# Optimization experiments

Hardware: AMD Instinct MI355X
Metric: run time of the kernel (lower is better)

The kernel has to match this reference:

```python
import jax, jax.numpy as jnp
import numpy as np

K = 20  # neighbors

def _edgeconv(x, W, b):
    # x: [B, C, N]; W: [O, 2C]; b: [O]
    xt = jnp.swapaxes(x, 1, 2)                      # [B, N, C]
    # pairwise (negative squared) distance: -|xi|^2 - 2 xi.xj ... wait torch: -xx - inner - xx^T
    inner = -2.0 * jnp.einsum('bic,bjc->bij', xt, xt)   # [B, N, N]
    xx = jnp.sum(xt * xt, axis=-1)                       # [B, N]
    pd = -xx[:, None, :] - inner - xx[:, :, None]        # [B, N, N]
    _, idx = jax.lax.top_k(pd, K)                        # [B, N, K] nearest neighbors
    # gather neighbor features: feat[b,n,k,:] = xt[b, idx[b,n,k], :]
    feat = jnp.take_along_axis(xt[:, None, :, :],        # [B,1,N,C]
                               idx[:, :, :, None], axis=2)  # [B, N, K, C]
    center = xt[:, :, None, :]                           # [B, N, 1, C]
    edge = jnp.concatenate([feat - center,
                            jnp.broadcast_to(center, feat.shape)], axis=-1)  # [B,N,K,2C]
    # 1x1 conv == linear over channel dim, then LeakyReLU(0.2)
    h = jnp.einsum('bnkc,oc->bnko', edge, W) + b         # [B, N, K, O]
    h = jnp.where(h >= 0, h, 0.2 * h)
    out = jnp.max(h, axis=2)                             # [B, N, O] (max over neighbors)
    return jnp.swapaxes(out, 1, 2)                       # [B, O, N]

def setup_inputs() -> dict:
    key = jax.random.key(0)
    k1, k2, k3 = jax.random.split(key, 3)
    B, C, N, O = 8, 64, 4096, 128
    x = jax.random.normal(k1, (B, C, N), dtype=jnp.float32)
    W = jax.random.normal(k2, (O, 2 * C), dtype=jnp.float32) * (1.0 / np.sqrt(2 * C))
    b = jax.random.normal(k3, (O,), dtype=jnp.float32) * 0.01
    return {"x": x, "W": W, "b": b}

def reference(x, W, b):
    return _edgeconv(x, W, b)
```

## Files before the change

kernel.cpp:

```cpp
#include <hip/hip_runtime.h>

#define BB 8
#define CC 64
#define OO 128
#define NN 4096
#define KNN 20
#define NT 256
#define NG 64
#define RING 9
#define TRIG 5
#define SPLITW 192
#define WSPL 384
#define TILEB (16 * SPLITW * 2)

typedef short bf16x8 __attribute__((ext_vector_type(8)));
typedef float f32x4 __attribute__((ext_vector_type(4)));
typedef const __attribute__((address_space(1))) unsigned int* gas_ptr;
typedef __attribute__((address_space(3))) unsigned int* las_ptr;

#define REP20(F, P) F(P,0) F(P,1) F(P,2) F(P,3) F(P,4) F(P,5) F(P,6) F(P,7) \
    F(P,8) F(P,9) F(P,10) F(P,11) F(P,12) F(P,13) F(P,14) F(P,15) F(P,16)   \
    F(P,17) F(P,18) F(P,19)

#define TS_DECL(P,k) float P##m##k = 1e30f; int P##p##k = -1;
#define TS_REPL(P,k)                                                        \
  { const bool _h = (P##kpos == (k));                                       \
    P##m##k = _h ? _d : P##m##k;                                            \
    P##p##k = _h ? _j : P##p##k; }

#define TS_N(vd, xd, va, xa, vb, xb)                                        \
  { const bool _g = (vb) > (va); vd = _g ? (vb) : (va); xd = _g ? (xb) : (xa); }

#define TS_TREE(P)                                                          \
  { float t0,t1,t2,t3,t4,t5,t6,t7,t8,t9; int y0,y1,y2,y3,y4,y5,y6,y7,y8,y9; \
    TS_N(t0,y0, P##m0,0,  P##m1,1)   TS_N(t1,y1, P##m2,2,  P##m3,3)         \
    TS_N(t2,y2, P##m4,4,  P##m5,5)   TS_N(t3,y3, P##m6,6,  P##m7,7)         \
    TS_N(t4,y4, P##m8,8,  P##m9,9)   TS_N(t5,y5, P##m10,10, P##m11,11)      \
    TS_N(t6,y6, P##m12,12, P##m13,13) TS_N(t7,y7, P##m14,14, P##m15,15)     \
    TS_N(t8,y8, P##m16,16, P##m17,17) TS_N(t9,y9, P##m18,18, P##m19,19)     \
    float u0,u1,u2,u3,u4; int z0,z1,z2,z3,z4;                               \
    TS_N(u0,z0, t0,y0, t1,y1) TS_N(u1,z1, t2,y2, t3,y3)                     \
    TS_N(u2,z2, t4,y4, t5,y5) TS_N(u3,z3, t6,y6, t7,y7)                     \
    TS_N(u4,z4, t8,y8, t9,y9)                                               \
    float w0,w1; int q0,q1;                                                 \
    TS_N(w0,q0, u0,z0, u1,z1) TS_N(w1,q1, u2,z2, u3,z3)                     \
    float e0; int r0;                                                       \
    TS_N(e0,r0, w0,q0, w1,q1)                                               \
    TS_N(P##kmax, P##kpos, e0,r0, u4,z4) }

#define TS_INS(P, dval, jval)                                               \
  { const float _d = (dval); const int _j = (jval);                         \
    REP20(TS_REPL, P)                                                       \
    TS_TREE(P) }

#define RT_UPDATE                                                           \
  { const int _s1 = __builtin_amdgcn_ds_swizzle(__float_as_int(A_kmax), 0x101F); \
    const float _m1 = fminf(A_kmax, __int_as_float(_s1));                   \
    const int _s2 = __builtin_amdgcn_ds_swizzle(__float_as_int(_m1), 0x201F); \
    rt = fminf(_m1, __int_as_float(_s2)); }

#define MSW(a, b)                                                           \
  { const bool _s = (A_m##b < A_m##a) ||                                    \
                    ((A_m##b == A_m##a) && (A_p##b < A_p##a));              \
    const float _fa = _s ? A_m##b : A_m##a;                                 \
    const float _fb = _s ? A_m##a : A_m##b;                                 \
    const int _ia = _s ? A_p##b : A_p##a;                                   \
    const int _ib = _s ? A_p##a : A_p##b;                                   \
    A_m##a = _fa; A_m##b = _fb; A_p##a = _ia; A_p##b = _ib; }

#define SRND_E MSW(0,1) MSW(2,3) MSW(4,5) MSW(6,7) MSW(8,9) MSW(10,11)      \
    MSW(12,13) MSW(14,15) MSW(16,17) MSW(18,19)
#define SRND_O MSW(1,2) MSW(3,4) MSW(5,6) MSW(7,8) MSW(9,10) MSW(11,12)     \
    MSW(13,14) MSW(15,16) MSW(17,18)
#define SORT20 SRND_E SRND_O SRND_E SRND_O SRND_E SRND_O SRND_E SRND_O      \
    SRND_E SRND_O SRND_E SRND_O SRND_E SRND_O SRND_E SRND_O SRND_E SRND_O  \
    SRND_E SRND_O

__device__ __forceinline__ unsigned rne_bf16(float f) {
  const unsigned u = __float_as_uint(f);
  return (u + 0x7fffu + ((u >> 16) & 1u)) >> 16;
}

__global__ __launch_bounds__(128, 3) void xprep_kernel(
    const float* __restrict__ x, const float* __restrict__ W,
    float* __restrict__ xsq, unsigned short* __restrict__ xsp,
    unsigned short* __restrict__ Wsp) {
  const int b = blockIdx.y;
  const int n = blockIdx.x * 128 + threadIdx.x;

  if (b == 0) {
    const int t = threadIdx.x;
    const int o0 = blockIdx.x * 4;
#pragma unroll
    for (int oo = 0; oo < 4; ++oo) {
      const int o = o0 + oo;
      const float w = W[(size_t)o * (2 * CC) + t];
      const unsigned h = rne_bf16(w);
      const float r = w - __uint_as_float(h << 16);
      const unsigned m = rne_bf16(r);
      const float s = r - __uint_as_float(m << 16);
      const unsigned l = rne_bf16(s);
      unsigned short* row = Wsp + (size_t)o * WSPL;
      row[t] = (unsigned short)h;
      row[128 + t] = (unsigned short)m;
      row[256 + t] = (unsigned short)l;
    }
  }

  const float* xb = x + (size_t)b * CC * NN;

  float xr[CC];
  float sq = 0.f;
#pragma unroll
  for (int c = 0; c < CC; ++c) {
    xr[c] = xb[(size_t)c * NN + n];
    sq = fmaf(xr[c], xr[c], sq);
  }
  xsq[(size_t)b * NN + n] = sq;

  unsigned* srow = (unsigned*)(xsp + ((size_t)b * NN + n) * SPLITW);
#pragma unroll
  for (int c = 0; c < CC; c += 2) {
    const unsigned h0 = rne_bf16(xr[c]), h1 = rne_bf16(xr[c + 1]);
    const float r0 = xr[c] - __uint_as_float(h0 << 16);
    const float r1 = xr[c + 1] - __uint_as_float(h1 << 16);
    const unsigned m0 = rne_bf16(r0), m1 = rne_bf16(r1);
    const float s0 = r0 - __uint_as_float(m0 << 16);
    const float s1 = r1 - __uint_as_float(m1 << 16);
    const unsigned l0 = rne_bf16(s0), l1 = rne_bf16(s1);
    srow[c / 2] = h0 | (h1 << 16);
    srow[32 + c / 2] = m0 | (m1 << 16);
    srow[64 + c / 2] = l0 | (l1 << 16);
  }
}

#define MFMA6(ACC, B0, B1, B2, B3, B4, B5)                                  \
  f32x4 ACC;                                                                \
  { f32x4 a0 = {0.f,0.f,0.f,0.f}; f32x4 a1 = {0.f,0.f,0.f,0.f};             \
    f32x4 a2 = {0.f,0.f,0.f,0.f}; f32x4 a3 = {0.f,0.f,0.f,0.f};             \
    a0 = __builtin_amdgcn_mfma_f32_16x16x32_bf16(Ah0, B0, a0, 0, 0, 0);     \
    a1 = __builtin_amdgcn_mfma_f32_16x16x32_bf16(Ah1, B1, a1, 0, 0, 0);     \
    a2 = __builtin_amdgcn_mfma_f32_16x16x32_bf16(Ah0, B2, a2, 0, 0, 0);     \
    a3 = __builtin_amdgcn_mfma_f32_16x16x32_bf16(Ah1, B3, a3, 0, 0, 0);     \
    a0 = __builtin_amdgcn_mfma_f32_16x16x32_bf16(Am0, B0, a0, 0, 0, 0);     \
    a1 = __builtin_amdgcn_mfma_f32_16x16x32_bf16(Am1, B1, a1, 0, 0, 0);     \
    a2 = __builtin_amdgcn_mfma_f32_16x16x32_bf16(Ah0, B4, a2, 0, 0, 0);     \
    a3 = __builtin_amdgcn_mfma_f32_16x16x32_bf16(Ah1, B5, a3, 0, 0, 0);     \
    a0 = __builtin_amdgcn_mfma_f32_16x16x32_bf16(Al0, B0, a0, 0, 0, 0);     \
    a1 = __builtin_amdgcn_mfma_f32_16x16x32_bf16(Al1, B1, a1, 0, 0, 0);     \
    a2 = __builtin_amdgcn_mfma_f32_16x16x32_bf16(Am0, B2, a2, 0, 0, 0);     \
    a3 = __builtin_amdgcn_mfma_f32_16x16x32_bf16(Am1, B3, a3, 0, 0, 0);     \
    ACC = (a0 + a1) + (a2 + a3); }

#define STAGEG(G, BUF)                                                      \
  { const char* tb = (const char*)xspB + (size_t)(4 * (G) + wv) * TILEB + gof; \
    char* lb = (char*)(BUF) + wv * 6144;                                    \
    __builtin_amdgcn_global_load_lds((gas_ptr)(const void*)(tb), (las_ptr)(void*)(lb), 16, 0, 0); \
    __builtin_amdgcn_global_load_lds((gas_ptr)(const void*)(tb + 64), (las_ptr)(void*)(lb + 1024), 16, 0, 0); \
    __builtin_amdgcn_global_load_lds((gas_ptr)(const void*)(tb + 128), (las_ptr)(void*)(lb + 2048), 16, 0, 0); \
    __builtin_amdgcn_global_load_lds((gas_ptr)(const void*)(tb + 192), (las_ptr)(void*)(lb + 3072), 16, 0, 0); \
    __builtin_amdgcn_global_load_lds((gas_ptr)(const void*)(tb + 256), (las_ptr)(void*)(lb + 4096), 16, 0, 0); \
    __builtin_amdgcn_global_load_lds((gas_ptr)(const void*)(tb + 320), (las_ptr)(void*)(lb + 5120), 16, 0, 0); }

#define TILE_MFMA_L(LBUF, BUF)                                              \
  { const char* bb = (const char*)(LBUF) + c16;                             \
    const bf16x8 Bh0 = *(const bf16x8*)(bb + (q + 0) * 256);                \
    const bf16x8 Bh1 = *(const bf16x8*)(bb + (q + 4) * 256);                \
    const bf16x8 Bm0 = *(const bf16x8*)(bb + (q + 8) * 256);                \
    const bf16x8 Bm1 = *(const bf16x8*)(bb + (q + 12) * 256);               \
    const bf16x8 Bl0 = *(const bf16x8*)(bb + (q + 16) * 256);               \
    const bf16x8 Bl1 = *(const bf16x8*)(bb + (q + 20) * 256);               \
    f32x4 ac0 = {0.f, 0.f, 0.f, 0.f};                                       \
    f32x4 ac1 = {0.f, 0.f, 0.f, 0.f};                                       \
    f32x4 ac2 = {0.f, 0.f, 0.f, 0.f};                                       \
    f32x4 ac3 = {0.f, 0.f, 0.f, 0.f};                                       \
    ac0 = __builtin_amdgcn_mfma_f32_16x16x32_bf16(Ah0, Bh0, ac0, 0, 0, 0);  \
    ac1 = __builtin_amdgcn_mfma_f32_16x16x32_bf16(Ah1, Bh1, ac1, 0, 0, 0);  \
    ac2 = __builtin_amdgcn_mfma_f32_16x16x32_bf16(Ah0, Bm0, ac2, 0, 0, 0);  \
    ac3 = __builtin_amdgcn_mfma_f32_16x16x32_bf16(Ah1, Bm1, ac3, 0, 0, 0);  \
    ac0 = __builtin_amdgcn_mfma_f32_16x16x32_bf16(Am0, Bh0, ac0, 0, 0, 0);  \
    ac1 = __builtin_amdgcn_mfma_f32_16x16x32_bf16(Am1, Bh1, ac1, 0, 0, 0);  \
    ac2 = __builtin_amdgcn_mfma_f32_16x16x32_bf16(Ah0, Bl0, ac2, 0, 0, 0);  \
    ac3 = __builtin_amdgcn_mfma_f32_16x16x32_bf16(Ah1, Bl1, ac3, 0, 0, 0);  \
    ac0 = __builtin_amdgcn_mfma_f32_16x16x32_bf16(Al0, Bh0, ac0, 0, 0, 0);  \
    ac1 = __builtin_amdgcn_mfma_f32_16x16x32_bf16(Al1, Bh1, ac1, 0, 0, 0);  \
    ac2 = __builtin_amdgcn_mfma_f32_16x16x32_bf16(Am0, Bm0, ac2, 0, 0, 0);  \
    ac3 = __builtin_amdgcn_mfma_f32_16x16x32_bf16(Am1, Bm1, ac3, 0, 0, 0);  \
    const f32x4 acc = (ac0 + ac1) + (ac2 + ac3);                            \
    float* bw = &bounce[BUF][wv][0];                                        \
    bw[(q * 4 + 0) * 20 + c] = acc[0];                                      \
    bw[(q * 4 + 1) * 20 + c] = acc[1];                                      \
    bw[(q * 4 + 2) * 20 + c] = acc[2];                                      \
    bw[(q * 4 + 3) * 20 + c] = acc[3]; }

#define TILE_VALS(T, BUF)                                                   \
  const float* br = &bounce[BUF][wv][myrow * 20 + 4 * g];                   \
  const f32x4 dots = *(const f32x4*)br;                                     \
  const float4 xx = *(const float4*)(xsqb + (T) * 16 + 4 * g);              \
  const float d0 = fmaf(-2.f, dots[0], xx.x);                               \
  const float d1 = fmaf(-2.f, dots[1], xx.y);                               \
  const float d2 = fmaf(-2.f, dots[2], xx.z);                               \
  const float d3 = fmaf(-2.f, dots[3], xx.w);                               \
  const int jb = (T) * 16 + 4 * g;

#define TILE_SELF(T, BUF, K0, K1, K2, K3)                                   \
  { TILE_VALS(T, BUF)                                                       \
    A_m##K0 = d0; A_p##K0 = jb;                                             \
    A_m##K1 = d1; A_p##K1 = jb + 1;                                         \
    A_m##K2 = d2; A_p##K2 = jb + 2;                                         \
    A_m##K3 = d3; A_p##K3 = jb + 3; }

#define TILE_SEL(T, BUF)                                                    \
  { TILE_VALS(T, BUF)                                                       \
    if (d0 <= rt) { myring[cnt] = make_float2(d0, __int_as_float(jb)); ++cnt; } \
    if (d1 <= rt) { myring[cnt] = make_float2(d1, __int_as_float(jb + 1)); ++cnt; } \
    if (d2 <= rt) { myring[cnt] = make_float2(d2, __int_as_float(jb + 2)); ++cnt; } \
    if (d3 <= rt) { myring[cnt] = make_float2(d3, __int_as_float(jb + 3)); ++cnt; } \
    if (__ballot(cnt >= TRIG)) {                                            \
      for (int _k = 0; _k < cnt; ++_k) {                                    \
        const float2 e = myring[_k];                                        \
        if (e.x < A_kmax) { TS_INS(A_, e.x, __float_as_int(e.y)) }          \
      }                                                                     \
      cnt = 0;                                                              \
    }                                                                       \
    RT_UPDATE }

__global__ __launch_bounds__(256, 2) void knn_kernel(
    const unsigned short* __restrict__ xsp, const float* __restrict__ xsq,
    const unsigned short* __restrict__ Wsp, const float* __restrict__ bias,
    unsigned short* __restrict__ Ab16, float* __restrict__ Q,
    int* __restrict__ idxf) {
  __shared__ unsigned short Bbuf0[4 * TILEB / 2];
  __shared__ unsigned short Bbuf1[4 * TILEB / 2];
  __shared__ float bounce[2][4][16 * 20];
  __shared__ float2 ring[256][RING];

  const int b = blockIdx.y;
  const int wv = threadIdx.x >> 6;
  const int lane = threadIdx.x & 63;
  const int q = lane >> 4;
  const int c = lane & 15;
  const int c16 = c * 16;
  const int gof = c * 384 + q * 16;
  const int ibase = blockIdx.x * 64 + wv * 16;
  const int myrow = q * 4 + (c & 3);
  const int g = c >> 2;
  const int isel = ibase + myrow;

  const unsigned short* xspB = xsp + (size_t)b * NN * SPLITW;
  const float* xsqb = xsq + (size_t)b * NN;

  const unsigned short* arow = xspB + (size_t)(ibase + c) * SPLITW + q * 8;
  const bf16x8 Ah0 = *(const bf16x8*)(arow);
  const bf16x8 Ah1 = *(const bf16x8*)(arow + 32);
  const bf16x8 Am0 = *(const bf16x8*)(arow + 64);
  const bf16x8 Am1 = *(const bf16x8*)(arow + 96);
  const bf16x8 Al0 = *(const bf16x8*)(arow + 128);
  const bf16x8 Al1 = *(const bf16x8*)(arow + 160);

  REP20(TS_DECL, A_)
  float A_kmax = 1e30f; int A_kpos = 0;
  float rt = 1e30f;
  float2* myring = ring[threadIdx.x];
  int cnt = 0;

  STAGEG(0, Bbuf0)
  __syncthreads();
  STAGEG(1, Bbuf1)
  TILE_MFMA_L(Bbuf0 + 0 * 3072, 0)
  TILE_MFMA_L(Bbuf0 + 1 * 3072, 1) TILE_SELF(0, 0, 0, 1, 2, 3)
  TILE_MFMA_L(Bbuf0 + 2 * 3072, 0) TILE_SELF(1, 1, 4, 5, 6, 7)
  TILE_MFMA_L(Bbuf0 + 3 * 3072, 1) TILE_SELF(2, 0, 8, 9, 10, 11)
  __syncthreads();
  STAGEG(2, Bbuf0)
  TILE_MFMA_L(Bbuf1 + 0 * 3072, 0) TILE_SELF(3, 1, 12, 13, 14, 15)
  TILE_MFMA_L(Bbuf1 + 1 * 3072, 1) TILE_SELF(4, 0, 16, 17, 18, 19)
  TS_TREE(A_)
  RT_UPDATE
  TILE_MFMA_L(Bbuf1 + 2 * 3072, 0) TILE_SEL(5, 1)
  TILE_MFMA_L(Bbuf1 + 3 * 3072, 1) TILE_SEL(6, 0)
  __syncthreads();

  for (int G = 2; G < NG - 1; ++G) {
    unsigned short* cur = (G & 1) ? Bbuf1 : Bbuf0;
    unsigned short* nxt = (G & 1) ? Bbuf0 : Bbuf1;
    STAGEG(G + 1, nxt)
    const int t0 = 4 * G;
    TILE_MFMA_L(cur + 0 * 3072, 0) TILE_SEL(t0 - 1, 1)
    TILE_MFMA_L(cur + 1 * 3072, 1) TILE_SEL(t0, 0)
    TILE_MFMA_L(cur + 2 * 3072, 0) TILE_SEL(t0 + 1, 1)
    TILE_MFMA_L(cur + 3 * 3072, 1) TILE_SEL(t0 + 2, 0)
    __syncthreads();
  }

  TILE_MFMA_L(Bbuf1 + 0 * 3072, 0) TILE_SEL(251, 1)
  TILE_MFMA_L(Bbuf1 + 1 * 3072, 1) TILE_SEL(252, 0)
  TILE_MFMA_L(Bbuf1 + 2 * 3072, 0) TILE_SEL(253, 1)
  TILE_MFMA_L(Bbuf1 + 3 * 3072, 1) TILE_SEL(254, 0)
  TILE_SEL(255, 1)

  for (int _k = 0; _k < cnt; ++_k) {
    const float2 e = myring[_k];
    if (e.x < A_kmax) { TS_INS(A_, e.x, __float_as_int(e.y)) }
  }

  __syncthreads();
  {
    SORT20
    float2* dumpw = (float2*)((wv & 2) ? (char*)Bbuf1 + (wv & 1) * 10752
                                       : (char*)Bbuf0 + (wv & 1) * 10752);
    float2* mydump = dumpw + lane * 21;
#define MG_DUMP(P, k) mydump[k] = make_float2(P##m##k, __int_as_float(P##p##k));
    REP20(MG_DUMP, A_)
#undef MG_DUMP
    const int srow = q * 16 + (c & 3);
    const float2* l0 = dumpw + (size_t)(srow + 0) * 21;
    const float2* l1 = dumpw + (size_t)(srow + 4) * 21;
    const float2* l2 = dumpw + (size_t)(srow + 8) * 21;
    const float2* l3 = dumpw + (size_t)(srow + 12) * 21;
    int c0 = 0, c1 = 0, c2 = 0, c3 = 0;
    float2 h0 = l0[0], h1 = l1[0], h2 = l2[0], h3 = l3[0];
    const size_t obase = (size_t)b * KNN * NN + isel;
    for (int k = 0; k < KNN; ++k) {
      const bool s01 =
          (h1.x < h0.x) ||
          ((h1.x == h0.x) && (__float_as_int(h1.y) < __float_as_int(h0.y)));
      const float2 m01 = s01 ? h1 : h0;
      const bool s23 =
          (h3.x < h2.x) ||
          ((h3.x == h2.x) && (__float_as_int(h3.y) < __float_as_int(h2.y)));
      const float2 m23 = s23 ? h3 : h2;
      const bool sF =
          (m23.x < m01.x) ||
          ((m23.x == m01.x) && (__float_as_int(m23.y) < __float_as_int(m01.y)));
      const float2 mm = sF ? m23 : m01;
      if (g == 0) idxf[obase + (size_t)k * NN] = __float_as_int(mm.y);
      const int w = sF ? (s23 ? 3 : 2) : (s01 ? 1 : 0);
      c0 += (w == 0); c1 += (w == 1); c2 += (w == 2); c3 += (w == 3);
      const float2 n0 = l0[c0], n1 = l1[c1], n2 = l2[c2], n3 = l3[c3];
      const float2 inf2 = make_float2(1e30f, __int_as_float(0x7fffffff));
      h0 = (c0 < KNN) ? n0 : inf2;
      h1 = (c1 < KNN) ? n1 : inf2;
      h2 = (c2 < KNN) ? n2 : inf2;
      h3 = (c3 < KNN) ? n3 : inf2;
    }
  }

  {
    unsigned short* Ab = Ab16 + (size_t)b * NN * OO;
    float* Qb = Q + (size_t)b * NN * OO;
#pragma unroll 2
    for (int ot = 0; ot < 8; ++ot) {
      const unsigned short* wrow = Wsp + (size_t)(ot * 16 + c) * WSPL + q * 8;
      const bf16x8 Ph0 = *(const bf16x8*)(wrow);
      const bf16x8 Ph1 = *(const bf16x8*)(wrow + 32);
      const bf16x8 Pm0 = *(const bf16x8*)(wrow + 128);
      const bf16x8 Pm1 = *(const bf16x8*)(wrow + 160);
      const bf16x8 Pl0 = *(const bf16x8*)(wrow + 256);
      const bf16x8 Pl1 = *(const bf16x8*)(wrow + 288);
      MFMA6(accP, Ph0, Ph1, Pm0, Pm1, Pl0, Pl1)
      const bf16x8 Gh0 = *(const bf16x8*)(wrow + 64);
      const bf16x8 Gh1 = *(const bf16x8*)(wrow + 96);
      const bf16x8 Gm0 = *(const bf16x8*)(wrow + 192);
      const bf16x8 Gm1 = *(const bf16x8*)(wrow + 224);
      const bf16x8 Gl0 = *(const bf16x8*)(wrow + 320);
      const bf16x8 Gl1 = *(const bf16x8*)(wrow + 352);
      MFMA6(accG, Gh0, Gh1, Gm0, Gm1, Gl0, Gl1)

      const float bv = bias[ot * 16 + c];
#pragma unroll
      for (int i = 0; i < 4; ++i) {
        const size_t row = (size_t)(ibase + q * 4 + i);
        const float p = accP[i];
        Ab[row * OO + ot * 16 + c] = (unsigned short)rne_bf16(p);
        Qb[row * OO + ot * 16 + c] = accG[i] - p + bv;
      }
    }
  }
}

__global__ __launch_bounds__(512) void gather_kernel(
    const unsigned short* __restrict__ Ab16, const float* __restrict__ Q,
    const int* __restrict__ idxf, float* __restrict__ out) {
  __shared__ int jidx[KNN][32];
  __shared__ float ob[32][OO + 1];

  const int b = blockIdx.y;
  const int n0 = blockIdx.x * 32;
  const int t = threadIdx.x;
  const int p = t & 31;
  const int h = t >> 5;

  if (t < KNN * 32) {
    const int k = t >> 5, ii = t & 31;
    jidx[k][ii] = idxf[((size_t)b * KNN + k) * NN + n0 + ii];
  }
  if (t + 512 < KNN * 32) {
    const int e = t + 512;
    const int k = e >> 5, ii = e & 31;
    jidx[k][ii] = idxf[((size_t)b * KNN + k) * NN + n0 + ii];
  }
  __syncthreads();

  const unsigned short* Ab = Ab16 + (size_t)b * NN * OO;
  const float* Qb = Q + (size_t)b * NN * OO;

  for (int ii = h * 2; ii < h * 2 + 2; ++ii) {
    float m0 = -1e30f, m1 = -1e30f, m2 = -1e30f, m3 = -1e30f;
#pragma unroll
    for (int k = 0; k < KNN; ++k) {
      const uint2 v =
          *(const uint2*)(Ab + (size_t)jidx[k][ii] * OO + 4 * p);
      m0 = fmaxf(m0, __uint_as_float(v.x << 16));
      m1 = fmaxf(m1, __uint_as_float(v.x & 0xFFFF0000u));
      m2 = fmaxf(m2, __uint_as_float(v.y << 16));
      m3 = fmaxf(m3, __uint_as_float(v.y & 0xFFFF0000u));
    }
    const float4 qv = *(const float4*)(Qb + (size_t)(n0 + ii) * OO + 4 * p);
    const float h0 = m0 + qv.x;
    const float h1 = m1 + qv.y;
    const float h2 = m2 + qv.z;
    const float h3 = m3 + qv.w;
    ob[ii][4 * p + 0] = (h0 >= 0.f) ? h0 : 0.2f * h0;
    ob[ii][4 * p + 1] = (h1 >= 0.f) ? h1 : 0.2f * h1;
    ob[ii][4 * p + 2] = (h2 >= 0.f) ? h2 : 0.2f * h2;
    ob[ii][4 * p + 3] = (h3 >= 0.f) ? h3 : 0.2f * h3;
  }
  __syncthreads();

  float* ou = out + (size_t)b * OO * NN;
  for (int e = t; e < 32 * OO; e += 512) {
    const int ii = e & 31, oo = e >> 5;
    ou[(size_t)oo * NN + n0 + ii] = ob[ii][oo];
  }
}

extern "C" void kernel_launch(void* const* d_in, const int* in_sizes, int n_in,
                              void* d_out, int out_size, void* d_ws,
                              size_t ws_size, hipStream_t stream) {
  (void)in_sizes;
  (void)n_in;
  (void)out_size;
  (void)ws_size;
  const float* x = (const float*)d_in[0];
  const float* W = (const float*)d_in[1];
  const float* bias = (const float*)d_in[2];
  float* out = (float*)d_out;

  char* ws = (char*)d_ws;
  size_t off = 0;
  unsigned short* Ab16 = (unsigned short*)(ws + off);
  off += (size_t)BB * NN * OO * 2;
  float* Q = (float*)(ws + off);
  off += (size_t)BB * NN * OO * 4;
  float* xsq = (float*)(ws + off);
  off += (size_t)BB * NN * 4;
  unsigned short* xsp = (unsigned short*)(ws + off);
  off += (size_t)BB * NN * SPLITW * 2;
  int* idxf = (int*)(ws + off);
  off += (size_t)BB * KNN * NN * 4;
  unsigned short* Wsp = (unsigned short*)(ws + off);
  off += (size_t)OO * WSPL * 2;

  xprep_kernel<<<dim3(NN / 128, BB), 128, 0, stream>>>(x, W, xsq, xsp, Wsp);
  knn_kernel<<<dim3(NN / 64, BB), 256, 0, stream>>>(xsp, xsq, Wsp, bias,
                                                    Ab16, Q, idxf);
  gather_kernel<<<dim3(NN / 32, BB), 512, 0, stream>>>(Ab16, Q, idxf, out);
}
```

Measured before the change: 439.2 us.

## Load kNN B tiles directly from global into registers, dropping LDS staging

Replaces the block-wide global_load_lds double-buffered staging of candidate-point tiles with per-wave direct global loads into two register sets (A/B ping-pong) that are prefetched one tile ahead. This removes the per-group __syncthreads barriers and the LDS round-trip, and shrinks shared memory so more blocks may fit per CU. The trade-off is that every wave now issues its own global loads, with no sharing across waves and less latency hiding than the LDS pipeline. More live vector registers are also needed for the prefetched tiles. A dedicated dump buffer replaces the reuse of the staging LDS for the final merge.

```diff
diff --git a/kernel.cpp b/kernel.cpp
--- a/kernel.cpp
+++ b/kernel.cpp
@@ -6,17 +6,13 @@
 #define NN 4096
 #define KNN 20
 #define NT 256
-#define NG 64
 #define RING 9
 #define TRIG 5
 #define SPLITW 192
 #define WSPL 384
-#define TILEB (16 * SPLITW * 2)
 
 typedef short bf16x8 __attribute__((ext_vector_type(8)));
 typedef float f32x4 __attribute__((ext_vector_type(4)));
-typedef const __attribute__((address_space(1))) unsigned int* gas_ptr;
-typedef __attribute__((address_space(3))) unsigned int* las_ptr;
 
 #define REP20(F, P) F(P,0) F(P,1) F(P,2) F(P,3) F(P,4) F(P,5) F(P,6) F(P,7) \
     F(P,8) F(P,9) F(P,10) F(P,11) F(P,12) F(P,13) F(P,14) F(P,15) F(P,16)   \
@@ -152,40 +148,33 @@
     a3 = __builtin_amdgcn_mfma_f32_16x16x32_bf16(Am1, B3, a3, 0, 0, 0);     \
     ACC = (a0 + a1) + (a2 + a3); }
 
-#define STAGEG(G, BUF)                                                      \
-  { const char* tb = (const char*)xspB + (size_t)(4 * (G) + wv) * TILEB + gof; \
-    char* lb = (char*)(BUF) + wv * 6144;                                    \
-    __builtin_amdgcn_global_load_lds((gas_ptr)(const void*)(tb), (las_ptr)(void*)(lb), 16, 0, 0); \
-    __builtin_amdgcn_global_load_lds((gas_ptr)(const void*)(tb + 64), (las_ptr)(void*)(lb + 1024), 16, 0, 0); \
-    __builtin_amdgcn_global_load_lds((gas_ptr)(const void*)(tb + 128), (las_ptr)(void*)(lb + 2048), 16, 0, 0); \
-    __builtin_amdgcn_global_load_lds((gas_ptr)(const void*)(tb + 192), (las_ptr)(void*)(lb + 3072), 16, 0, 0); \
-    __builtin_amdgcn_global_load_lds((gas_ptr)(const void*)(tb + 256), (las_ptr)(void*)(lb + 4096), 16, 0, 0); \
-    __builtin_amdgcn_global_load_lds((gas_ptr)(const void*)(tb + 320), (las_ptr)(void*)(lb + 5120), 16, 0, 0); }
-
-#define TILE_MFMA_L(LBUF, BUF)                                              \
-  { const char* bb = (const char*)(LBUF) + c16;                             \
-    const bf16x8 Bh0 = *(const bf16x8*)(bb + (q + 0) * 256);                \
-    const bf16x8 Bh1 = *(const bf16x8*)(bb + (q + 4) * 256);                \
-    const bf16x8 Bm0 = *(const bf16x8*)(bb + (q + 8) * 256);                \
-    const bf16x8 Bm1 = *(const bf16x8*)(bb + (q + 12) * 256);               \
-    const bf16x8 Bl0 = *(const bf16x8*)(bb + (q + 16) * 256);               \
-    const bf16x8 Bl1 = *(const bf16x8*)(bb + (q + 20) * 256);               \
-    f32x4 ac0 = {0.f, 0.f, 0.f, 0.f};                                       \
+#define LB(S, T)                                                            \
+  { const unsigned short* brow =                                            \
+        xspB + (size_t)((T) * 16 + c) * SPLITW + q * 8;                     \
+    Bh0##S = *(const bf16x8*)(brow);                                        \
+    Bh1##S = *(const bf16x8*)(brow + 32);                                   \
+    Bm0##S = *(const bf16x8*)(brow + 64);                                   \
+    Bm1##S = *(const bf16x8*)(brow + 96);                                   \
+    Bl0##S = *(const bf16x8*)(brow + 128);                                  \
+    Bl1##S = *(const bf16x8*)(brow + 160); }
+
+#define MM(S, BUF)                                                          \
+  { f32x4 ac0 = {0.f, 0.f, 0.f, 0.f};                                       \
     f32x4 ac1 = {0.f, 0.f, 0.f, 0.f};                                       \
     f32x4 ac2 = {0.f, 0.f, 0.f, 0.f};                                       \
     f32x4 ac3 = {0.f, 0.f, 0.f, 0.f};                                       \
-    ac0 = __builtin_amdgcn_mfma_f32_16x16x32_bf16(Ah0, Bh0, ac0, 0, 0, 0);  \
-    ac1 = __builtin_amdgcn_mfma_f32_16x16x32_bf16(Ah1, Bh1, ac1, 0, 0, 0);  \
-    ac2 = __builtin_amdgcn_mfma_f32_16x16x32_bf16(Ah0, Bm0, ac2, 0, 0, 0);  \
-    ac3 = __builtin_amdgcn_mfma_f32_16x16x32_bf16(Ah1, Bm1, ac3, 0, 0, 0);  \
-    ac0 = __builtin_amdgcn_mfma_f32_16x16x32_bf16(Am0, Bh0, ac0, 0, 0, 0);  \
-    ac1 = __builtin_amdgcn_mfma_f32_16x16x32_bf16(Am1, Bh1, ac1, 0, 0, 0);  \
-    ac2 = __builtin_amdgcn_mfma_f32_16x16x32_bf16(Ah0, Bl0, ac2, 0, 0, 0);  \
-    ac3 = __builtin_amdgcn_mfma_f32_16x16x32_bf16(Ah1, Bl1, ac3, 0, 0, 0);  \
-    ac0 = __builtin_amdgcn_mfma_f32_16x16x32_bf16(Al0, Bh0, ac0, 0, 0, 0);  \
-    ac1 = __builtin_amdgcn_mfma_f32_16x16x32_bf16(Al1, Bh1, ac1, 0, 0, 0);  \
-    ac2 = __builtin_amdgcn_mfma_f32_16x16x32_bf16(Am0, Bm0, ac2, 0, 0, 0);  \
-    ac3 = __builtin_amdgcn_mfma_f32_16x16x32_bf16(Am1, Bm1, ac3, 0, 0, 0);  \
+    ac0 = __builtin_amdgcn_mfma_f32_16x16x32_bf16(Ah0, Bh0##S, ac0, 0, 0, 0); \
+    ac1 = __builtin_amdgcn_mfma_f32_16x16x32_bf16(Ah1, Bh1##S, ac1, 0, 0, 0); \
+    ac2 = __builtin_amdgcn_mfma_f32_16x16x32_bf16(Ah0, Bm0##S, ac2, 0, 0, 0); \
+    ac3 = __builtin_amdgcn_mfma_f32_16x16x32_bf16(Ah1, Bm1##S, ac3, 0, 0, 0); \
+    ac0 = __builtin_amdgcn_mfma_f32_16x16x32_bf16(Am0, Bh0##S, ac0, 0, 0, 0); \
+    ac1 = __builtin_amdgcn_mfma_f32_16x16x32_bf16(Am1, Bh1##S, ac1, 0, 0, 0); \
+    ac2 = __builtin_amdgcn_mfma_f32_16x16x32_bf16(Ah0, Bl0##S, ac2, 0, 0, 0); \
+    ac3 = __builtin_amdgcn_mfma_f32_16x16x32_bf16(Ah1, Bl1##S, ac3, 0, 0, 0); \
+    ac0 = __builtin_amdgcn_mfma_f32_16x16x32_bf16(Al0, Bh0##S, ac0, 0, 0, 0); \
+    ac1 = __builtin_amdgcn_mfma_f32_16x16x32_bf16(Al1, Bh1##S, ac1, 0, 0, 0); \
+    ac2 = __builtin_amdgcn_mfma_f32_16x16x32_bf16(Am0, Bm0##S, ac2, 0, 0, 0); \
+    ac3 = __builtin_amdgcn_mfma_f32_16x16x32_bf16(Am1, Bm1##S, ac3, 0, 0, 0); \
     const f32x4 acc = (ac0 + ac1) + (ac2 + ac3);                            \
     float* bw = &bounce[BUF][wv][0];                                        \
     bw[(q * 4 + 0) * 20 + c] = acc[0];                                      \
@@ -230,18 +219,15 @@
     const unsigned short* __restrict__ Wsp, const float* __restrict__ bias,
     unsigned short* __restrict__ Ab16, float* __restrict__ Q,
     int* __restrict__ idxf) {
-  __shared__ unsigned short Bbuf0[4 * TILEB / 2];
-  __shared__ unsigned short Bbuf1[4 * TILEB / 2];
   __shared__ float bounce[2][4][16 * 20];
   __shared__ float2 ring[256][RING];
+  __shared__ float2 dump[4][64 * 21];
 
   const int b = blockIdx.y;
   const int wv = threadIdx.x >> 6;
   const int lane = threadIdx.x & 63;
   const int q = lane >> 4;
   const int c = lane & 15;
-  const int c16 = c * 16;
-  const int gof = c * 384 + q * 16;
   const int ibase = blockIdx.x * 64 + wv * 16;
   const int myrow = q * 4 + (c & 3);
   const int g = c >> 2;
@@ -258,45 +244,41 @@
   const bf16x8 Al0 = *(const bf16x8*)(arow + 128);
   const bf16x8 Al1 = *(const bf16x8*)(arow + 160);
 
+  bf16x8 Bh0A, Bh1A, Bm0A, Bm1A, Bl0A, Bl1A;
+  bf16x8 Bh0B, Bh1B, Bm0B, Bm1B, Bl0B, Bl1B;
+
   REP20(TS_DECL, A_)
   float A_kmax = 1e30f; int A_kpos = 0;
   float rt = 1e30f;
   float2* myring = ring[threadIdx.x];
   int cnt = 0;
 
-  STAGEG(0, Bbuf0)
-  __syncthreads();
-  STAGEG(1, Bbuf1)
-  TILE_MFMA_L(Bbuf0 + 0 * 3072, 0)
-  TILE_MFMA_L(Bbuf0 + 1 * 3072, 1) TILE_SELF(0, 0, 0, 1, 2, 3)
-  TILE_MFMA_L(Bbuf0 + 2 * 3072, 0) TILE_SELF(1, 1, 4, 5, 6, 7)
-  TILE_MFMA_L(Bbuf0 + 3 * 3072, 1) TILE_SELF(2, 0, 8, 9, 10, 11)
-  __syncthreads();
-  STAGEG(2, Bbuf0)
-  TILE_MFMA_L(Bbuf1 + 0 * 3072, 0) TILE_SELF(3, 1, 12, 13, 14, 15)
-  TILE_MFMA_L(Bbuf1 + 1 * 3072, 1) TILE_SELF(4, 0, 16, 17, 18, 19)
+  LB(A, 0)
+  LB(B, 1)
+  MM(A, 0)
+  LB(A, 2)
+  MM(B, 1) TILE_SELF(0, 0, 0, 1, 2, 3)
+  LB(B, 3)
+  MM(A, 0) TILE_SELF(1, 1, 4, 5, 6, 7)
+  LB(A, 4)
+  MM(B, 1) TILE_SELF(2, 0, 8, 9, 10, 11)
+  LB(B, 5)
+  MM(A, 0) TILE_SELF(3, 1, 12, 13, 14, 15)
+  LB(A, 6)
+  MM(B, 1) TILE_SELF(4, 0, 16, 17, 18, 19)
   TS_TREE(A_)
   RT_UPDATE
-  TILE_MFMA_L(Bbuf1 + 2 * 3072, 0) TILE_SEL(5, 1)
-  TILE_MFMA_L(Bbuf1 + 3 * 3072, 1) TILE_SEL(6, 0)
-  __syncthreads();
-
-  for (int G = 2; G < NG - 1; ++G) {
-    unsigned short* cur = (G & 1) ? Bbuf1 : Bbuf0;
-    unsigned short* nxt = (G & 1) ? Bbuf0 : Bbuf1;
-    STAGEG(G + 1, nxt)
-    const int t0 = 4 * G;
-    TILE_MFMA_L(cur + 0 * 3072, 0) TILE_SEL(t0 - 1, 1)
-    TILE_MFMA_L(cur + 1 * 3072, 1) TILE_SEL(t0, 0)
-    TILE_MFMA_L(cur + 2 * 3072, 0) TILE_SEL(t0 + 1, 1)
-    TILE_MFMA_L(cur + 3 * 3072, 1) TILE_SEL(t0 + 2, 0)
-    __syncthreads();
-  }
-
-  TILE_MFMA_L(Bbuf1 + 0 * 3072, 0) TILE_SEL(251, 1)
-  TILE_MFMA_L(Bbuf1 + 1 * 3072, 1) TILE_SEL(252, 0)
-  TILE_MFMA_L(Bbuf1 + 2 * 3072, 0) TILE_SEL(253, 1)
-  TILE_MFMA_L(Bbuf1 + 3 * 3072, 1) TILE_SEL(254, 0)
+  LB(B, 7)
+  MM(A, 0) TILE_SEL(5, 1)
+
+  for (int t = 7; t < 255; t += 2) {
+    LB(A, t + 1)
+    MM(B, 1) TILE_SEL(t - 1, 0)
+    LB(B, t + 2)
+    MM(A, 0) TILE_SEL(t, 1)
+  }
+
+  MM(B, 1) TILE_SEL(254, 0)
   TILE_SEL(255, 1)
 
   for (int _k = 0; _k < cnt; ++_k) {
@@ -304,11 +286,9 @@
     if (e.x < A_kmax) { TS_INS(A_, e.x, __float_as_int(e.y)) }
   }
 
-  __syncthreads();
   {
     SORT20
-    float2* dumpw = (float2*)((wv & 2) ? (char*)Bbuf1 + (wv & 1) * 10752
-                                       : (char*)Bbuf0 + (wv & 1) * 10752);
+    float2* dumpw = &dump[wv][0];
     float2* mydump = dumpw + lane * 21;
 #define MG_DUMP(P, k) mydump[k] = make_float2(P##m##k, __int_as_float(P##p##k));
     REP20(MG_DUMP, A_)
```

Result: slower. 481.8 us (+9.7%).
